# Performance work log

Measured on AMD Instinct MI355X. Metric: run time of the kernel, lower is better.

The kernel has to match this reference:

```python
import jax, jax.numpy as jnp
import numpy as np

QMAX = 127.0  # 2**(bits-1) - 1 for bits=8, signed symmetric


def _quantize_signed_symmetric(t):
    # per-tensor symmetric: scale = max|t| / qmax, q = clamp(round(t/scale))
    scale = jnp.max(jnp.abs(t)) / QMAX
    q = jnp.clip(jnp.round(t / scale), -QMAX, QMAX)
    return q, scale


def setup_inputs() -> dict:
    key = jax.random.key(0)
    k1, k2, k3 = jax.random.split(key, 3)
    N, D_IN, D_OUT = 16384, 1024, 1024
    x = jax.random.normal(k1, (N, D_IN), dtype=jnp.float32)
    weight = jax.random.normal(k2, (D_OUT, D_IN), dtype=jnp.float32) * 0.02
    bias = jax.random.normal(k3, (D_OUT,), dtype=jnp.float32) * 0.01
    return {"x": x, "weight": weight, "bias": bias}


def reference(x, weight, bias):
    # weight quantization (cached in torch; recomputed here, same math)
    qw, w_scale = _quantize_signed_symmetric(weight)
    qw_t = qw.astype(jnp.int32).T            # [D_IN, D_OUT]
    # activation quantization
    qx, x_scale = _quantize_signed_symmetric(x)
    qx = qx.astype(jnp.int32)                # [N, D_IN]
    # int32 matmul, then per-tensor dequant + bias
    acc = qx @ qw_t                          # int32 [N, D_OUT]
    y = acc.astype(jnp.float32) * (x_scale * w_scale)
    return y + bias
```

## Files before the change

### kernel.cpp

```cpp
#include <hip/hip_runtime.h>

#define QMAX 127.0f

typedef int int4v __attribute__((ext_vector_type(4)));
typedef float float4v __attribute__((ext_vector_type(4)));

__global__ void absmax2_kernel(const float4* __restrict__ px, int n4x,
                               const float4* __restrict__ pw, int n4w,
                               int gx, int* __restrict__ amax) {
    const float4* p; int n4; int* out; int nb, bid;
    if ((int)blockIdx.x < gx) { p = px; n4 = n4x; out = amax + 0; nb = gx; bid = blockIdx.x; }
    else { p = pw; n4 = n4w; out = amax + 1; nb = gridDim.x - gx; bid = blockIdx.x - gx; }
    float m = 0.f;
    int stride = nb * blockDim.x;
    for (int i = bid * blockDim.x + threadIdx.x; i < n4; i += stride) {
        float4 v = p[i];
        m = fmaxf(m, fmaxf(fmaxf(fabsf(v.x), fabsf(v.y)),
                           fmaxf(fabsf(v.z), fabsf(v.w))));
    }
    for (int off = 32; off; off >>= 1) m = fmaxf(m, __shfl_down(m, off, 64));
    __shared__ float sm[4];
    if ((threadIdx.x & 63) == 0) sm[threadIdx.x >> 6] = m;
    __syncthreads();
    if (threadIdx.x == 0) {
        float b = fmaxf(fmaxf(sm[0], sm[1]), fmaxf(sm[2], sm[3]));
        atomicMax(out, (int)__float_as_uint(b));
    }
}

__device__ __forceinline__ int qone(float v, float s) {
    float q = fminf(fmaxf(rintf(v / s), -QMAX), QMAX);
    return (int)q;
}
__device__ __forceinline__ int qpack4(float4 v, float s) {
    return (qone(v.x, s) & 255) | ((qone(v.y, s) & 255) << 8) |
           ((qone(v.z, s) & 255) << 16) | ((qone(v.w, s) & 255) << 24);
}

__global__ void quant2_kernel(const float4* __restrict__ sx, int4v* __restrict__ dx, int n16x,
                              const float4* __restrict__ sw, int4v* __restrict__ dw, int n16w,
                              int gx, int kshift, int KC, const int* __restrict__ amax) {
    const float4* src; int n16, nb, bid; float scale; int isw;
    if ((int)blockIdx.x < gx) {
        src = sx; n16 = n16x; nb = gx; bid = blockIdx.x; isw = 0;
        scale = __uint_as_float((unsigned)amax[0]) / QMAX;
    } else {
        src = sw; n16 = n16w; nb = gridDim.x - gx; bid = blockIdx.x - gx; isw = 1;
        scale = __uint_as_float((unsigned)amax[1]) / QMAX;
    }
    int stride = nb * blockDim.x;
    for (int i = bid * blockDim.x + threadIdx.x; i < n16; i += stride) {
        float4 v0 = src[4 * i + 0];
        float4 v1 = src[4 * i + 1];
        float4 v2 = src[4 * i + 2];
        float4 v3 = src[4 * i + 3];
        int4v o = { qpack4(v0, scale), qpack4(v1, scale),
                    qpack4(v2, scale), qpack4(v3, scale) };
        if (!isw) {
            dx[i] = o;
        } else {
            int n = i >> kshift;
            int kg = i & ((1 << kshift) - 1);
            int kc = kg >> 2, q = kg & 3;
            int g = n >> 4, r = n & 15;
            dw[(g * KC + kc) * 64 + q * 16 + r] = o;
        }
    }
}

typedef const __attribute__((address_space(1))) char glob_char;
typedef __attribute__((address_space(3))) char lds_char;

__device__ __forceinline__ void gload16(const char* g, char* l) {
    __builtin_amdgcn_global_load_lds((glob_char*)g, (lds_char*)l, 16, 0, 0);
}

__global__ __launch_bounds__(512, 2) void gemm_i8_kernel(
        const char* __restrict__ qa, const char* __restrict__ qb,
        const float4* __restrict__ bias4, const int* __restrict__ amax,
        float* __restrict__ out, int M, int N, int K) {
    extern __shared__ char sA[];

    const int KC = K >> 6;
    const int tid = threadIdx.x;
    const int lane = tid & 63;
    const int w = tid >> 6;
    const int m0 = blockIdx.x * 64;
    const int kb = __builtin_ctz(K);

    const int rounds = (K >> 3) >> 2;
    for (int R = 0; R < rounds; ++R) {
        const int C = R * 512 + tid;
        const int i = C >> kb;
        const int kc = (C & (K - 1)) >> 6;
        const int q = (C >> 4) & 3;
        const int r = C & 15;
        const char* src = qa + (size_t)(m0 + i * 16 + r) * K + kc * 64 + q * 16;
        gload16(src, sA + (size_t)C * 16);
    }
    __syncthreads();

    int4v acc[8][4];
    const int4v zero = {0, 0, 0, 0};
#pragma unroll
    for (int j = 0; j < 8; ++j)
#pragma unroll
        for (int i = 0; i < 4; ++i) acc[j][i] = zero;

    const int4v* sAv = (const int4v*)sA;
    const char* bbase = qb + (size_t)(w * 8) * KC * 1024 + lane * 16;

#define LOADB(Bb, kc)                                                        \
    do { _Pragma("unroll") for (int j = 0; j < 8; ++j)                       \
        Bb[j] = *(const int4v*)(bbase + ((size_t)j * KC + (kc)) * 1024);     \
    } while (0)
#define LOADA(Af, kc)                                                        \
    do { _Pragma("unroll") for (int i = 0; i < 4; ++i)                       \
        Af[i] = sAv[i * K + (kc) * 64 + lane];                               \
    } while (0)
#define MF(Bb, Af)                                                           \
    do { _Pragma("unroll") for (int j = 0; j < 8; ++j)                       \
        _Pragma("unroll") for (int i = 0; i < 4; ++i)                        \
            acc[j][i] = __builtin_amdgcn_mfma_i32_16x16x64_i8(               \
                Bb[j], Af[i], acc[j][i], 0, 0, 0);                           \
    } while (0)

    int4v B0[8], B1[8], Af[4];
    LOADB(B0, 0);
#pragma unroll 1
    for (int kc = 0; kc + 2 < KC; kc += 2) {
        LOADB(B1, kc + 1);
        LOADA(Af, kc);
        MF(B0, Af);
        LOADB(B0, kc + 2);
        LOADA(Af, kc + 1);
        MF(B1, Af);
    }
    LOADB(B1, KC - 1);
    LOADA(Af, KC - 2);
    MF(B0, Af);
    LOADA(Af, KC - 1);
    MF(B1, Af);

    const float sc = (__uint_as_float((unsigned)amax[0]) / QMAX) *
                     (__uint_as_float((unsigned)amax[1]) / QMAX);
    const int quad = lane >> 4;
    const int rbase = m0 + (lane & 15);
    const int cb4 = w * 32;
#pragma unroll
    for (int j = 0; j < 8; ++j) {
        const float4 bv = bias4[cb4 + j * 4 + quad];
#pragma unroll
        for (int i = 0; i < 4; ++i) {
            const int row = rbase + i * 16;
            float4v v;
            v[0] = (float)acc[j][i][0] * sc + bv.x;
            v[1] = (float)acc[j][i][1] * sc + bv.y;
            v[2] = (float)acc[j][i][2] * sc + bv.z;
            v[3] = (float)acc[j][i][3] * sc + bv.w;
            *((float4v*)(out + (size_t)row * N) + cb4 + j * 4 + quad) = v;
        }
    }
}

extern "C" void kernel_launch(void* const* d_in, const int* in_sizes, int n_in,
                              void* d_out, int out_size, void* d_ws, size_t ws_size,
                              hipStream_t stream) {
    const float* x = (const float*)d_in[0];
    const float* w = (const float*)d_in[1];
    const float* bias = (const float*)d_in[2];
    float* out = (float*)d_out;

    const int xn = in_sizes[0];
    const int wn = in_sizes[1];
    const int N = in_sizes[2];
    const int K = wn / N;
    const int M = xn / K;
    const int KC = K >> 6;
    const int kshift = __builtin_ctz(K >> 4);

    int* amax = (int*)d_ws;
    char* qx = (char*)d_ws + 1024;
    char* qw = qx + (size_t)M * K;

    const int GAX = 2048, GAW = 256;
    absmax2_kernel<<<GAX + GAW, 256, 0, stream>>>(
        (const float4*)x, xn / 4, (const float4*)w, wn / 4, GAX, amax);

    const int GQX = 4096, GQW = 256;
    quant2_kernel<<<GQX + GQW, 256, 0, stream>>>(
        (const float4*)x, (int4v*)qx, xn / 16,
        (const float4*)w, (int4v*)qw, wn / 16, GQX, kshift, KC, amax);

    gemm_i8_kernel<<<M / 64, 512, 64 * K, stream>>>(
        qx, qw, (const float4*)bias, amax, out, M, N, K);
}
```

Baseline: 174.7 us.

## Fuse activation quantization into GEMM A-tile load, drop int8 x buffer

```diff
diff --git a/kernel.cpp b/kernel.cpp
--- a/kernel.cpp
+++ b/kernel.cpp
@@ -5,26 +5,38 @@
 typedef int int4v __attribute__((ext_vector_type(4)));
 typedef float float4v __attribute__((ext_vector_type(4)));
 
+__device__ __forceinline__ float amax4(float4 v) {
+    return fmaxf(fmaxf(fabsf(v.x), fabsf(v.y)), fmaxf(fabsf(v.z), fabsf(v.w)));
+}
+
 __global__ void absmax2_kernel(const float4* __restrict__ px, int n4x,
                                const float4* __restrict__ pw, int n4w,
                                int gx, int* __restrict__ amax) {
     const float4* p; int n4; int* out; int nb, bid;
     if ((int)blockIdx.x < gx) { p = px; n4 = n4x; out = amax + 0; nb = gx; bid = blockIdx.x; }
     else { p = pw; n4 = n4w; out = amax + 1; nb = gridDim.x - gx; bid = blockIdx.x - gx; }
-    float m = 0.f;
-    int stride = nb * blockDim.x;
-    for (int i = bid * blockDim.x + threadIdx.x; i < n4; i += stride) {
-        float4 v = p[i];
-        m = fmaxf(m, fmaxf(fmaxf(fabsf(v.x), fabsf(v.y)),
-                           fmaxf(fabsf(v.z), fabsf(v.w))));
+    const int S = nb * blockDim.x;
+    int i = bid * blockDim.x + threadIdx.x;
+    float a = 0.f, b = 0.f, c = 0.f, d = 0.f;
+    for (; i + 3 * S < n4; i += 4 * S) {
+        float4 v0 = p[i];
+        float4 v1 = p[i + S];
+        float4 v2 = p[i + 2 * S];
+        float4 v3 = p[i + 3 * S];
+        a = fmaxf(a, amax4(v0));
+        b = fmaxf(b, amax4(v1));
+        c = fmaxf(c, amax4(v2));
+        d = fmaxf(d, amax4(v3));
     }
+    for (; i < n4; i += S) a = fmaxf(a, amax4(p[i]));
+    float m = fmaxf(fmaxf(a, b), fmaxf(c, d));
     for (int off = 32; off; off >>= 1) m = fmaxf(m, __shfl_down(m, off, 64));
     __shared__ float sm[4];
     if ((threadIdx.x & 63) == 0) sm[threadIdx.x >> 6] = m;
     __syncthreads();
     if (threadIdx.x == 0) {
-        float b = fmaxf(fmaxf(sm[0], sm[1]), fmaxf(sm[2], sm[3]));
-        atomicMax(out, (int)__float_as_uint(b));
+        float bm = fmaxf(fmaxf(sm[0], sm[1]), fmaxf(sm[2], sm[3]));
+        atomicMax(out, (int)__float_as_uint(bm));
     }
 }
 
@@ -37,46 +49,28 @@
            ((qone(v.z, s) & 255) << 16) | ((qone(v.w, s) & 255) << 24);
 }
 
-__global__ void quant2_kernel(const float4* __restrict__ sx, int4v* __restrict__ dx, int n16x,
-                              const float4* __restrict__ sw, int4v* __restrict__ dw, int n16w,
-                              int gx, int kshift, int KC, const int* __restrict__ amax) {
-    const float4* src; int n16, nb, bid; float scale; int isw;
-    if ((int)blockIdx.x < gx) {
-        src = sx; n16 = n16x; nb = gx; bid = blockIdx.x; isw = 0;
-        scale = __uint_as_float((unsigned)amax[0]) / QMAX;
-    } else {
-        src = sw; n16 = n16w; nb = gridDim.x - gx; bid = blockIdx.x - gx; isw = 1;
-        scale = __uint_as_float((unsigned)amax[1]) / QMAX;
-    }
-    int stride = nb * blockDim.x;
-    for (int i = bid * blockDim.x + threadIdx.x; i < n16; i += stride) {
-        float4 v0 = src[4 * i + 0];
-        float4 v1 = src[4 * i + 1];
-        float4 v2 = src[4 * i + 2];
-        float4 v3 = src[4 * i + 3];
+__global__ void quantw_kernel(const float4* __restrict__ sw, int4v* __restrict__ dw,
+                              int n16w, int kshift, int KC,
+                              const int* __restrict__ amax) {
+    const float scale = __uint_as_float((unsigned)amax[1]) / QMAX;
+    const int stride = gridDim.x * blockDim.x;
+    for (int i = blockIdx.x * blockDim.x + threadIdx.x; i < n16w; i += stride) {
+        float4 v0 = sw[4 * i + 0];
+        float4 v1 = sw[4 * i + 1];
+        float4 v2 = sw[4 * i + 2];
+        float4 v3 = sw[4 * i + 3];
         int4v o = { qpack4(v0, scale), qpack4(v1, scale),
                     qpack4(v2, scale), qpack4(v3, scale) };
-        if (!isw) {
-            dx[i] = o;
-        } else {
-            int n = i >> kshift;
-            int kg = i & ((1 << kshift) - 1);
-            int kc = kg >> 2, q = kg & 3;
-            int g = n >> 4, r = n & 15;
-            dw[(g * KC + kc) * 64 + q * 16 + r] = o;
-        }
+        const int n = i >> kshift;
+        const int kg = i & ((1 << kshift) - 1);
+        const int kc = kg >> 2, q = kg & 3;
+        const int g = n >> 4, r = n & 15;
+        dw[(g * KC + kc) * 64 + q * 16 + r] = o;
     }
 }
 
-typedef const __attribute__((address_space(1))) char glob_char;
-typedef __attribute__((address_space(3))) char lds_char;
-
-__device__ __forceinline__ void gload16(const char* g, char* l) {
-    __builtin_amdgcn_global_load_lds((glob_char*)g, (lds_char*)l, 16, 0, 0);
-}
-
 __global__ __launch_bounds__(512, 2) void gemm_i8_kernel(
-        const char* __restrict__ qa, const char* __restrict__ qb,
+        const float* __restrict__ x, const char* __restrict__ qb,
         const float4* __restrict__ bias4, const int* __restrict__ amax,
         float* __restrict__ out, int M, int N, int K) {
     extern __shared__ char sA[];
@@ -86,17 +80,26 @@
     const int lane = tid & 63;
     const int w = tid >> 6;
     const int m0 = blockIdx.x * 64;
-    const int kb = __builtin_ctz(K);
 
-    const int rounds = (K >> 3) >> 2;
-    for (int R = 0; R < rounds; ++R) {
-        const int C = R * 512 + tid;
-        const int i = C >> kb;
-        const int kc = (C & (K - 1)) >> 6;
-        const int q = (C >> 4) & 3;
-        const int r = C & 15;
-        const char* src = qa + (size_t)(m0 + i * 16 + r) * K + kc * 64 + q * 16;
-        gload16(src, sA + (size_t)C * 16);
+    const float xs = __uint_as_float((unsigned)amax[0]) / QMAX;
+    int4v* sAv_w = (int4v*)sA;
+    const int kcs = __builtin_ctz(KC);
+    const int PPW = KC >> 1;
+#pragma unroll 2
+    for (int p = 0; p < PPW; ++p) {
+        const int pair = w * PPW + p;
+        const int i = pair >> kcs;
+        const int kc = pair & (KC - 1);
+        const int row = m0 + i * 16 + (lane & 15);
+        const int k0 = kc * 64 + (lane >> 4) * 16;
+        const float4* src = (const float4*)(x + (size_t)row * K + k0);
+        float4 v0 = src[0];
+        float4 v1 = src[1];
+        float4 v2 = src[2];
+        float4 v3 = src[3];
+        int4v o = { qpack4(v0, xs), qpack4(v1, xs),
+                    qpack4(v2, xs), qpack4(v3, xs) };
+        sAv_w[i * K + kc * 64 + lane] = o;
     }
     __syncthreads();
 
@@ -180,18 +183,15 @@
     const int kshift = __builtin_ctz(K >> 4);
 
     int* amax = (int*)d_ws;
-    char* qx = (char*)d_ws + 1024;
-    char* qw = qx + (size_t)M * K;
+    char* qw = (char*)d_ws + 1024;
 
     const int GAX = 2048, GAW = 256;
     absmax2_kernel<<<GAX + GAW, 256, 0, stream>>>(
         (const float4*)x, xn / 4, (const float4*)w, wn / 4, GAX, amax);
 
-    const int GQX = 4096, GQW = 256;
-    quant2_kernel<<<GQX + GQW, 256, 0, stream>>>(
-        (const float4*)x, (int4v*)qx, xn / 16,
-        (const float4*)w, (int4v*)qw, wn / 16, GQX, kshift, KC, amax);
+    quantw_kernel<<<256, 256, 0, stream>>>(
+        (const float4*)w, (int4v*)qw, wn / 16, kshift, KC, amax);
 
     gemm_i8_kernel<<<M / 64, 512, 64 * K, stream>>>(
-        qx, qw, (const float4*)bias, amax, out, M, N, K);
+        x, qw, (const float4*)bias, amax, out, M, N, K);
 }
```

New measurement: 166.4 us. -4.8%, faster.
